# Performance work log

Hardware: AMD Instinct MI355X
Metric: run time of the kernel (lower is better)

Reference implementation:

```python
import jax, jax.numpy as jnp
import numpy as np

# IR-Net EDE surrogate-gradient constants (ir_1w1a.IRConv2d defaults)
K = 10.0
T = 0.1
BN_EPS = 1e-5

@jax.custom_vjp
def binary_quantize(x):
    return jnp.sign(x)

def _bq_fwd(x):
    return jnp.sign(x), x

def _bq_bwd(x, g):
    # grad = k * t * (1 - tanh(x*t)^2) * g   (IR-Net BinaryQuantize.backward)
    return (K * T * (1.0 - jnp.tanh(x * T) ** 2) * g,)

binary_quantize.defvjp(_bq_fwd, _bq_bwd)


def setup_inputs() -> dict:
    key = jax.random.key(0)
    k1, k2 = jax.random.split(key, 2)
    return {
        "x": jax.random.normal(k1, (32, 256, 56, 56), dtype=jnp.float32),
        "weight": jax.random.normal(k2, (256, 256, 3, 3), dtype=jnp.float32) * 0.05,
        "gamma": jnp.ones((256,), dtype=jnp.float32),
        "beta": jnp.zeros((256,), dtype=jnp.float32),
    }


def _convalg(x, weight, gamma, beta):
    co = weight.shape[0]
    wf = weight.reshape(co, -1)
    # per-output-channel standardization of weights
    bw = weight - wf.mean(-1).reshape(co, 1, 1, 1)
    std = jnp.std(bw.reshape(co, -1), axis=-1, ddof=1).reshape(co, 1, 1, 1)  # torch unbiased std
    bw = bw / std
    # detached power-of-2 per-channel scale: sw = 2^round(log2(mean|bw|))
    sw = jax.lax.stop_gradient(
        2.0 ** jnp.round(jnp.log2(jnp.abs(bw).reshape(co, -1).mean(-1)))
    ).reshape(co, 1, 1, 1)
    bwq = binary_quantize(bw) * sw   # binarized, scaled weights {-sw, +sw}
    ba = binary_quantize(x)          # binarized activations {-1, +1}
    y = jax.lax.conv_general_dilated(
        ba, bwq,
        window_strides=(1, 1),
        padding=((1, 1), (1, 1)),
        dimension_numbers=("NCHW", "OIHW", "NCHW"),
    )
    # BatchNorm2d, training-mode forward (batch statistics, biased variance)
    mean = y.mean(axis=(0, 2, 3), keepdims=True)
    var = y.var(axis=(0, 2, 3), keepdims=True)
    yn = (y - mean) * jax.lax.rsqrt(var + BN_EPS)
    yn = yn * gamma.reshape(1, -1, 1, 1) + beta.reshape(1, -1, 1, 1)
    # Hardtanh
    return jnp.clip(yn, -1.0, 1.0)


def reference(x, weight, gamma, beta):
    return _convalg(x, weight, gamma, beta)
```

## Files before the change

### kernel.cpp

```cpp
#include <hip/hip_runtime.h>
#include <math.h>

#define HH 56
#define WW 56
#define NB 32
#define CC 256
#define PIX 3136
#define M_TOT 100352
#define PADH 58
#define PADW 58
#define ACTQ_BYTES ((size_t)NB*PADH*PADW*CC)
#define WQ_BYTES ((size_t)9*CC*CC)
#define SBUF_BYTES ((size_t)M_TOT*CC*2)
#define BM 128
#define BN 128

typedef unsigned int u32;
typedef unsigned long long u64;
typedef int v4i __attribute__((ext_vector_type(4)));

typedef const __attribute__((address_space(1))) unsigned int* as1_u32p;
typedef __attribute__((address_space(3))) unsigned int* as3_u32p;
#define GLOAD_LDS16(g, l) \
  __builtin_amdgcn_global_load_lds((as1_u32p)(g), (as3_u32p)(l), 16, 0, 0)

__global__ __launch_bounds__(256) void pack_weights_i8(
    const float* __restrict__ wt, signed char* __restrict__ wq,
    float* __restrict__ swv,
    long long* __restrict__ sumS, long long* __restrict__ sumSS) {
  int co = blockIdx.x;
  int t  = threadIdx.x;
  int lane = t & 63, wid = t >> 6;

  float wv[9];
  const float* wp = wt + ((size_t)co*CC + t)*9;
  double psum = 0.0;
#pragma unroll
  for (int k = 0; k < 9; ++k) { wv[k] = wp[k]; psum += (double)wv[k]; }

  __shared__ double redm[4];
#pragma unroll
  for (int off = 32; off > 0; off >>= 1) psum += __shfl_xor(psum, off);
  if (lane == 0) redm[wid] = psum;
  __syncthreads();
  double mean = (redm[0]+redm[1]+redm[2]+redm[3]) * (1.0/2304.0);

  double pabs = 0.0, psq = 0.0;
#pragma unroll
  for (int k = 0; k < 9; ++k) {
    double d = (double)wv[k] - mean;
    pabs += fabs(d);
    psq  += d*d;
  }
#pragma unroll
  for (int off = 32; off > 0; off >>= 1) {
    pabs += __shfl_xor(pabs, off);
    psq  += __shfl_xor(psq,  off);
  }
  __shared__ double reda[4], redq[4];
  if (lane == 0) { reda[wid] = pabs; redq[wid] = psq; }
  __syncthreads();
  if (t == 0) {
    double sa = reda[0]+reda[1]+reda[2]+reda[3];
    double sq = redq[0]+redq[1]+redq[2]+redq[3];
    double stdv = sqrt(sq / 2303.0);
    double mabs = (sa * (1.0/2304.0)) / stdv;
    swv[co] = (float)exp2(rint(log2(mabs)));
    sumS[co]  = 0;
    sumSS[co] = 0;
  }
#pragma unroll
  for (int k = 0; k < 9; ++k)
    wq[((size_t)k*CC + co)*CC + t] =
        (((double)wv[k] - mean) > 0.0) ? (signed char)1 : (signed char)-1;
}

__global__ __launch_bounds__(256) void pack_acts_i8(
    const float* __restrict__ x, signed char* __restrict__ actq) {
  int n = blockIdx.y, tile = blockIdx.x;
  int lane = threadIdx.x & 63, cw = threadIdx.x >> 6;
  int pp = tile*64 + lane;
  if (pp >= PADH*PADW) return;
  int ph = pp / PADW, pw = pp - ph*PADW;
  signed char* dst = actq + ((size_t)(n*PADH + ph)*PADW + pw)*CC + cw*64;
  if (ph == 0 || ph == PADH-1 || pw == 0 || pw == PADW-1) {
    uint4 z = make_uint4(0u, 0u, 0u, 0u);
#pragma unroll
    for (int q = 0; q < 4; ++q) ((uint4*)dst)[q] = z;
    return;
  }
  int h = ph - 1, w = pw - 1;
  const float* xp = x + ((size_t)(n*CC + cw*64))*PIX + h*WW + w;
  u32 wrd[16];
#pragma unroll
  for (int c16 = 0; c16 < 16; ++c16) {
    u32 v = 0;
#pragma unroll
    for (int b = 0; b < 4; ++b) {
      float f = xp[(size_t)(c16*4 + b)*PIX];
      v |= (f > 0.0f ? 0x01u : 0xFFu) << (8*b);
    }
    wrd[c16] = v;
  }
#pragma unroll
  for (int q = 0; q < 4; ++q)
    ((uint4*)dst)[q] = make_uint4(wrd[4*q], wrd[4*q+1], wrd[4*q+2], wrd[4*q+3]);
}


#define STAGEM(SN, BUF) do {                                              \
    int tn_ = (SN) >> 2, kn_ = (SN) & 3;                                  \
    int aoff_ = ((tn_/3 - 1)*PADW + (tn_%3 - 1))*CC + kn_*64;             \
    int boff_ = tn_*65536 + kn_*64;                                       \
    char* nb_ = (char*)lds + (BUF)*16384;                                 \
    GLOAD_LDS16(pA0 + aoff_, nb_ + ldst);                                 \
    GLOAD_LDS16(pA1 + aoff_, nb_ + 4096 + ldst);                          \
    GLOAD_LDS16(pB0 + boff_, nb_ + 8192 + ldst);                          \
    GLOAD_LDS16(pB1 + boff_, nb_ + 12288 + ldst);                         \
  } while (0)

#define STEPM(S, BUF, WTXT, DOSTAGE) do {                                 \
    asm volatile("s_waitcnt " WTXT ::: "memory");                         \
    __builtin_amdgcn_s_barrier();                                         \
    const char* cb_ = (const char*)lds + (BUF)*16384;                     \
    v4i af[4], bf[4];                                                     \
    _Pragma("unroll")                                                     \
    for (int i = 0; i < 4; ++i)                                           \
      af[i] = *(const v4i*)(cb_ + (ar0 + i*16 + lm)*64 + rdo);            \
    _Pragma("unroll")                                                     \
    for (int j = 0; j < 4; ++j)                                           \
      bf[j] = *(const v4i*)(cb_ + 8192 + (bc0 + j*16 + lm)*64 + rdo);     \
    asm volatile("s_waitcnt lgkmcnt(0)" ::: "memory");                    \
    __builtin_amdgcn_s_barrier();                                         \
    if (DOSTAGE) { STAGEM((S) + 3, BUF); }                                \
    __builtin_amdgcn_s_setprio(1);                                        \
    _Pragma("unroll")                                                     \
    for (int i = 0; i < 4; ++i)                                           \
      _Pragma("unroll")                                                   \
      for (int j = 0; j < 4; ++j)                                         \
        acc[i][j] = __builtin_amdgcn_mfma_i32_16x16x64_i8(af[i], bf[j],   \
                                                          acc[i][j], 0, 0, 0); \
    __builtin_amdgcn_s_setprio(0);                                        \
  } while (0)

template <bool S16>
__global__ __launch_bounds__(256, 3) void bconv_mfma(
    const signed char* __restrict__ actq, const signed char* __restrict__ wq,
    short* __restrict__ s16out, float* __restrict__ f32out,
    u64* __restrict__ sumS, u64* __restrict__ sumSS) {
  __shared__ char lds[49152] __attribute__((aligned(16)));
  __shared__ int colS[128], colQ[128];

  int t = threadIdx.x;
  int lane = t & 63, wv = t >> 6;
  int lm = lane & 15, quad = lane >> 4;
  int ar0 = (wv & 1) * 64;
  int bc0 = (wv >> 1) * 64;
  int Mbase = blockIdx.x * BM;
  int n0 = blockIdx.y * BN;

  if (t < 128) { colS[t] = 0; colQ[t] = 0; }

  int r = t >> 2, c16 = t & 3;
  int cs = c16 ^ ((r >> 1) & 3);
  const signed char *pA0, *pA1;
  {
    int P = Mbase + r;
    int n_ = P / PIX, pl_ = P % PIX, h_ = pl_ / WW, w_ = pl_ % WW;
    pA0 = actq + ((size_t)(n_*PADH + h_+1)*PADW + (w_+1))*CC + cs*16;
    P += 64;
    n_ = P / PIX; pl_ = P % PIX; h_ = pl_ / WW; w_ = pl_ % WW;
    pA1 = actq + ((size_t)(n_*PADH + h_+1)*PADW + (w_+1))*CC + cs*16;
  }
  const signed char* pB0 = wq + (size_t)(n0 + r)*CC + cs*16;
  const signed char* pB1 = pB0 + 64*CC;
  int ldst = t*16;

  int rdo = (quad ^ ((lm >> 1) & 3)) * 16;

  v4i acc[4][4];
#pragma unroll
  for (int i = 0; i < 4; ++i)
#pragma unroll
    for (int j = 0; j < 4; ++j) acc[i][j] = 0;

  STAGEM(0, 0);
  STAGEM(1, 1);
  STAGEM(2, 2);

#pragma unroll 1
  for (int s = 0; s < 33; s += 3) {
    STEPM(s,     0, "vmcnt(8)", true);
    STEPM(s + 1, 1, "vmcnt(8)", true);
    STEPM(s + 2, 2, "vmcnt(8)", true);
  }
  STEPM(33, 0, "vmcnt(8)", false);
  STEPM(34, 1, "vmcnt(4)", false);
  STEPM(35, 2, "vmcnt(0)", false);

  int Sl[4] = {0,0,0,0}, Ql[4] = {0,0,0,0};
#pragma unroll
  for (int i = 0; i < 4; ++i) {
    int R = Mbase + ar0 + i*16 + quad*4;
    int nR = R / PIX, plR = R % PIX;
#pragma unroll
    for (int j = 0; j < 4; ++j) {
      int colo = n0 + bc0 + j*16 + lm;
      v4i a = acc[i][j];
      size_t idx = ((size_t)nR*CC + colo)*PIX + plR;
      if (S16) {
        int2 pk;
        pk.x = (a.x & 0xFFFF) | (a.y << 16);
        pk.y = (a.z & 0xFFFF) | (a.w << 16);
        *(int2*)(s16out + idx) = pk;
      } else {
        *(float4*)(f32out + idx) =
            make_float4((float)a.x, (float)a.y, (float)a.z, (float)a.w);
      }
      Sl[j] += a.x + a.y + a.z + a.w;
      Ql[j] += a.x*a.x + a.y*a.y + a.z*a.z + a.w*a.w;
    }
  }
#pragma unroll
  for (int j = 0; j < 4; ++j) {
    int S = Sl[j], Q = Ql[j];
    S += __shfl_xor(S, 16); S += __shfl_xor(S, 32);
    Q += __shfl_xor(Q, 16); Q += __shfl_xor(Q, 32);
    if (quad == 0) {
      atomicAdd(&colS[bc0 + j*16 + lm], S);
      atomicAdd(&colQ[bc0 + j*16 + lm], Q);
    }
  }
  __syncthreads();
  if (t < 128) {
    atomicAdd(&sumS[n0 + t], (u64)(long long)colS[t]);
    atomicAdd(&sumSS[n0 + t], (u64)(long long)colQ[t]);
  }
}

__global__ void finalize_stats(
    const long long* __restrict__ sumS, const long long* __restrict__ sumSS,
    const float* __restrict__ swv,
    const float* __restrict__ gamma, const float* __restrict__ beta,
    float* __restrict__ AB) {
  int c = threadIdx.x;
  double mu  = (double)sumS[c]  / (double)M_TOT;
  double var = (double)sumSS[c] / (double)M_TOT - mu*mu;
  double sw  = (double)swv[c];
  double inv = 1.0 / sqrt(sw*sw*var + 1e-5);
  double scale = (double)gamma[c] * sw * inv;
  double shift = (double)beta[c] - scale * mu;
  AB[c]      = (float)scale;
  AB[CC + c] = (float)shift;
}

__global__ __launch_bounds__(256) void bn_apply_s16(
    const short* __restrict__ s, float* __restrict__ out,
    const float* __restrict__ AB, int n8) {
  int i = blockIdx.x*256 + threadIdx.x;
  if (i >= n8) return;
  union { int4 v; short sh[8]; } u;
  u.v = ((const int4*)s)[i];
  int c = ((i*8) / PIX) & (CC-1);
  float a = AB[c], b = AB[CC + c];
  float4 o0, o1;
  o0.x = fminf(1.f, fmaxf(-1.f, (float)u.sh[0]*a + b));
  o0.y = fminf(1.f, fmaxf(-1.f, (float)u.sh[1]*a + b));
  o0.z = fminf(1.f, fmaxf(-1.f, (float)u.sh[2]*a + b));
  o0.w = fminf(1.f, fmaxf(-1.f, (float)u.sh[3]*a + b));
  o1.x = fminf(1.f, fmaxf(-1.f, (float)u.sh[4]*a + b));
  o1.y = fminf(1.f, fmaxf(-1.f, (float)u.sh[5]*a + b));
  o1.z = fminf(1.f, fmaxf(-1.f, (float)u.sh[6]*a + b));
  o1.w = fminf(1.f, fmaxf(-1.f, (float)u.sh[7]*a + b));
  ((float4*)out)[2*i]   = o0;
  ((float4*)out)[2*i+1] = o1;
}

__global__ __launch_bounds__(256) void bn_apply_f32(
    float* __restrict__ out, const float* __restrict__ AB, int n4) {
  int i = blockIdx.x*256 + threadIdx.x;
  if (i >= n4) return;
  float4 v = ((float4*)out)[i];
  int c = ((i*4) / PIX) & (CC-1);
  float a = AB[c], b = AB[CC + c];
  v.x = fminf(1.f, fmaxf(-1.f, v.x*a + b));
  v.y = fminf(1.f, fmaxf(-1.f, v.y*a + b));
  v.z = fminf(1.f, fmaxf(-1.f, v.z*a + b));
  v.w = fminf(1.f, fmaxf(-1.f, v.w*a + b));
  ((float4*)out)[i] = v;
}

extern "C" void kernel_launch(void* const* d_in, const int* in_sizes, int n_in,
                              void* d_out, int out_size, void* d_ws, size_t ws_size,
                              hipStream_t stream) {
  (void)in_sizes; (void)n_in; (void)out_size;
  const float* x     = (const float*)d_in[0];
  const float* wt    = (const float*)d_in[1];
  const float* gamma = (const float*)d_in[2];
  const float* beta  = (const float*)d_in[3];
  float* out = (float*)d_out;

  char* ws = (char*)d_ws;
  size_t off = 0;
  signed char* actq = (signed char*)(ws + off);
  off += ACTQ_BYTES;             off = (off + 255) & ~(size_t)255;
  signed char* wq = (signed char*)(ws + off);
  off += WQ_BYTES;               off = (off + 255) & ~(size_t)255;
  float* swv = (float*)(ws + off); off += 1024;
  float* AB  = (float*)(ws + off); off += 2048;
  long long* sumS  = (long long*)(ws + off); off += 2048;
  long long* sumSS = (long long*)(ws + off); off += 2048;
  off = (off + 255) & ~(size_t)255;
  short* sbuf = (short*)(ws + off);
  bool s16 = (ws_size >= off + SBUF_BYTES);

  pack_weights_i8<<<256, 256, 0, stream>>>(wt, wq, swv, sumS, sumSS);
  pack_acts_i8<<<dim3(53, NB), 256, 0, stream>>>(x, actq);
  if (s16) {
    bconv_mfma<true><<<dim3(M_TOT/BM, CC/BN), 256, 0, stream>>>(
        actq, wq, sbuf, nullptr, (u64*)sumS, (u64*)sumSS);
  } else {
    bconv_mfma<false><<<dim3(M_TOT/BM, CC/BN), 256, 0, stream>>>(
        actq, wq, nullptr, out, (u64*)sumS, (u64*)sumSS);
  }
  finalize_stats<<<1, 256, 0, stream>>>(sumS, sumSS, swv, gamma, beta, AB);
  if (s16) {
    bn_apply_s16<<<(M_TOT*CC/8 + 255)/256, 256, 0, stream>>>(
        sbuf, out, AB, M_TOT*CC/8);
  } else {
    bn_apply_f32<<<(M_TOT*CC/4 + 255)/256, 256, 0, stream>>>(
        out, AB, M_TOT*CC/4);
  }
}
```

Measured before the change: 162.0 us.

## Double-buffer MFMA register fragments to overlap LDS reads with MFMA

Restructures the main K-loop so each step reads the next stage's A/B fragments from LDS into a second register set while the MFMAs run on the current set. This removes one barrier per step and hides LDS read latency behind matrix math, with sched_barriers pinning the order. It costs extra VGPRs for the second fragment set, which may hurt occupancy under launch_bounds(256,3), and it changes the vmcnt wait accounting, which risks a race on the triple-buffered LDS.

```diff
diff --git a/kernel.cpp b/kernel.cpp
--- a/kernel.cpp
+++ b/kernel.cpp
@@ -119,28 +119,36 @@
     GLOAD_LDS16(pB1 + boff_, nb_ + 12288 + ldst);                         \
   } while (0)
 
-#define STEPM(S, BUF, WTXT, DOSTAGE) do {                                 \
+#define FRAGS_READ(NB_, NXTA, NXTB) do {                                  \
+    const char* cb_ = (const char*)lds + (NB_)*16384;                     \
+    _Pragma("unroll")                                                     \
+    for (int i_ = 0; i_ < 4; ++i_)                                        \
+      NXTA[i_] = *(const v4i*)(cb_ + (ar0 + i_*16 + lm)*64 + rdo);        \
+    _Pragma("unroll")                                                     \
+    for (int j_ = 0; j_ < 4; ++j_)                                        \
+      NXTB[j_] = *(const v4i*)(cb_ + 8192 + (bc0 + j_*16 + lm)*64 + rdo); \
+  } while (0)
+
+#define MFMA16(CURA, CURB) do {                                           \
+    __builtin_amdgcn_s_setprio(1);                                        \
+    _Pragma("unroll")                                                     \
+    for (int i_ = 0; i_ < 4; ++i_)                                        \
+      _Pragma("unroll")                                                   \
+      for (int j_ = 0; j_ < 4; ++j_)                                      \
+        acc[i_][j_] = __builtin_amdgcn_mfma_i32_16x16x64_i8(              \
+            CURA[i_], CURB[j_], acc[i_][j_], 0, 0, 0);                    \
+    __builtin_amdgcn_s_setprio(0);                                        \
+  } while (0)
+
+#define STEP(S, BUF, NBUF, CURA, CURB, NXTA, NXTB, WTXT, DOSTAGE) do {    \
     asm volatile("s_waitcnt " WTXT ::: "memory");                         \
     __builtin_amdgcn_s_barrier();                                         \
-    const char* cb_ = (const char*)lds + (BUF)*16384;                     \
-    v4i af[4], bf[4];                                                     \
-    _Pragma("unroll")                                                     \
-    for (int i = 0; i < 4; ++i)                                           \
-      af[i] = *(const v4i*)(cb_ + (ar0 + i*16 + lm)*64 + rdo);            \
-    _Pragma("unroll")                                                     \
-    for (int j = 0; j < 4; ++j)                                           \
-      bf[j] = *(const v4i*)(cb_ + 8192 + (bc0 + j*16 + lm)*64 + rdo);     \
+    __builtin_amdgcn_sched_barrier(0);                                    \
+    FRAGS_READ(NBUF, NXTA, NXTB);                                         \
+    if (DOSTAGE) { STAGEM((S) + 3, BUF); }                                \
+    MFMA16(CURA, CURB);                                                   \
     asm volatile("s_waitcnt lgkmcnt(0)" ::: "memory");                    \
-    __builtin_amdgcn_s_barrier();                                         \
-    if (DOSTAGE) { STAGEM((S) + 3, BUF); }                                \
-    __builtin_amdgcn_s_setprio(1);                                        \
-    _Pragma("unroll")                                                     \
-    for (int i = 0; i < 4; ++i)                                           \
-      _Pragma("unroll")                                                   \
-      for (int j = 0; j < 4; ++j)                                         \
-        acc[i][j] = __builtin_amdgcn_mfma_i32_16x16x64_i8(af[i], bf[j],   \
-                                                          acc[i][j], 0, 0, 0); \
-    __builtin_amdgcn_s_setprio(0);                                        \
+    __builtin_amdgcn_sched_barrier(0);                                    \
   } while (0)
 
 template <bool S16>
@@ -184,19 +192,33 @@
 #pragma unroll
     for (int j = 0; j < 4; ++j) acc[i][j] = 0;
 
+  v4i a0[4], b0[4], a1[4], b1[4];
+
   STAGEM(0, 0);
   STAGEM(1, 1);
   STAGEM(2, 2);
+  asm volatile("s_waitcnt vmcnt(8)" ::: "memory");
+  __builtin_amdgcn_s_barrier();
+  __builtin_amdgcn_sched_barrier(0);
+  FRAGS_READ(0, a0, b0);
+  asm volatile("s_waitcnt lgkmcnt(0)" ::: "memory");
+  __builtin_amdgcn_sched_barrier(0);
 
 #pragma unroll 1
-  for (int s = 0; s < 33; s += 3) {
-    STEPM(s,     0, "vmcnt(8)", true);
-    STEPM(s + 1, 1, "vmcnt(8)", true);
-    STEPM(s + 2, 2, "vmcnt(8)", true);
-  }
-  STEPM(33, 0, "vmcnt(8)", false);
-  STEPM(34, 1, "vmcnt(4)", false);
-  STEPM(35, 2, "vmcnt(0)", false);
+  for (int s6 = 0; s6 < 30; s6 += 6) {
+    STEP(s6+0, 0, 1, a0, b0, a1, b1, "vmcnt(4)", true);
+    STEP(s6+1, 1, 2, a1, b1, a0, b0, "vmcnt(4)", true);
+    STEP(s6+2, 2, 0, a0, b0, a1, b1, "vmcnt(4)", true);
+    STEP(s6+3, 0, 1, a1, b1, a0, b0, "vmcnt(4)", true);
+    STEP(s6+4, 1, 2, a0, b0, a1, b1, "vmcnt(4)", true);
+    STEP(s6+5, 2, 0, a1, b1, a0, b0, "vmcnt(4)", true);
+  }
+  STEP(30, 0, 1, a0, b0, a1, b1, "vmcnt(4)", true);
+  STEP(31, 1, 2, a1, b1, a0, b0, "vmcnt(4)", true);
+  STEP(32, 2, 0, a0, b0, a1, b1, "vmcnt(4)", true);
+  STEP(33, 0, 1, a1, b1, a0, b0, "vmcnt(4)", false);
+  STEP(34, 1, 2, a0, b0, a1, b1, "vmcnt(0)", false);
+  MFMA16(a1, b1);
 
   int Sl[4] = {0,0,0,0}, Ql[4] = {0,0,0,0};
 #pragma unroll
```

New measurement: 164.9 us. No clear change (+1.8%).

## Load weight fragments directly to registers and tile-major int16 intermediate layout

Applied to the files above, without the earlier changes.

The GEMM loop now stages only activations through LDS with a 3-slot ring and loads weight fragments straight from global memory into double-buffered registers. This drops the second barrier per step and halves LDS use. Occupancy hint drops from 3 to 2 blocks per CU. The int16 intermediate is written in a per-tile contiguous layout, and the BN apply kernel remaps indices back to NCHW, so the conv kernel's stores become contiguous while the scatter moves into the apply pass. Risks are uncoalesced direct weight loads, higher register pressure and a pipeline depth reduced from 3 stages to 2.

```diff
diff --git a/kernel.cpp b/kernel.cpp
--- a/kernel.cpp
+++ b/kernel.cpp
@@ -108,47 +108,50 @@
 }
 
 
-#define STAGEM(SN, BUF) do {                                              \
+#define STAGEA(SN) do {                                                   \
     int tn_ = (SN) >> 2, kn_ = (SN) & 3;                                  \
     int aoff_ = ((tn_/3 - 1)*PADW + (tn_%3 - 1))*CC + kn_*64;             \
-    int boff_ = tn_*65536 + kn_*64;                                       \
-    char* nb_ = (char*)lds + (BUF)*16384;                                 \
+    char* nb_ = (char*)lds + (((SN) % 3) << 13);                          \
     GLOAD_LDS16(pA0 + aoff_, nb_ + ldst);                                 \
     GLOAD_LDS16(pA1 + aoff_, nb_ + 4096 + ldst);                          \
-    GLOAD_LDS16(pB0 + boff_, nb_ + 8192 + ldst);                          \
-    GLOAD_LDS16(pB1 + boff_, nb_ + 12288 + ldst);                         \
   } while (0)
 
-#define STEPM(S, BUF, WTXT, DOSTAGE) do {                                 \
+#define LOADB(SN, BF) do {                                                \
+    int tn_ = (SN) >> 2, kn_ = (SN) & 3;                                  \
+    int boff_ = tn_*65536 + kn_*64;                                       \
+    BF[0] = *(const v4i*)(pBg + boff_);                                   \
+    BF[1] = *(const v4i*)(pBg + boff_ + 4096);                            \
+    BF[2] = *(const v4i*)(pBg + boff_ + 8192);                            \
+    BF[3] = *(const v4i*)(pBg + boff_ + 12288);                           \
+  } while (0)
+
+#define STEP(S, BCUR, BNXT, WTXT, DOA, DOB) do {                          \
     asm volatile("s_waitcnt " WTXT ::: "memory");                         \
     __builtin_amdgcn_s_barrier();                                         \
-    const char* cb_ = (const char*)lds + (BUF)*16384;                     \
-    v4i af[4], bf[4];                                                     \
+    __builtin_amdgcn_sched_barrier(0);                                    \
+    if (DOB) { LOADB((S) + 1, BNXT); }                                    \
+    if (DOA) { STAGEA((S) + 2); }                                         \
+    const char* cb_ = (const char*)lds + (((S) % 3) << 13);               \
+    v4i af[4];                                                            \
     _Pragma("unroll")                                                     \
-    for (int i = 0; i < 4; ++i)                                           \
-      af[i] = *(const v4i*)(cb_ + (ar0 + i*16 + lm)*64 + rdo);            \
-    _Pragma("unroll")                                                     \
-    for (int j = 0; j < 4; ++j)                                           \
-      bf[j] = *(const v4i*)(cb_ + 8192 + (bc0 + j*16 + lm)*64 + rdo);     \
-    asm volatile("s_waitcnt lgkmcnt(0)" ::: "memory");                    \
-    __builtin_amdgcn_s_barrier();                                         \
-    if (DOSTAGE) { STAGEM((S) + 3, BUF); }                                \
+    for (int i_ = 0; i_ < 4; ++i_)                                        \
+      af[i_] = *(const v4i*)(cb_ + (ar0 + i_*16 + lm)*64 + rdo);          \
     __builtin_amdgcn_s_setprio(1);                                        \
     _Pragma("unroll")                                                     \
-    for (int i = 0; i < 4; ++i)                                           \
+    for (int j_ = 0; j_ < 4; ++j_)                                        \
       _Pragma("unroll")                                                   \
-      for (int j = 0; j < 4; ++j)                                         \
-        acc[i][j] = __builtin_amdgcn_mfma_i32_16x16x64_i8(af[i], bf[j],   \
-                                                          acc[i][j], 0, 0, 0); \
+      for (int i_ = 0; i_ < 4; ++i_)                                      \
+        acc[i_][j_] = __builtin_amdgcn_mfma_i32_16x16x64_i8(              \
+            af[i_], BCUR[j_], acc[i_][j_], 0, 0, 0);                      \
     __builtin_amdgcn_s_setprio(0);                                        \
   } while (0)
 
 template <bool S16>
-__global__ __launch_bounds__(256, 3) void bconv_mfma(
+__global__ __launch_bounds__(256, 2) void bconv_mfma(
     const signed char* __restrict__ actq, const signed char* __restrict__ wq,
     short* __restrict__ s16out, float* __restrict__ f32out,
     u64* __restrict__ sumS, u64* __restrict__ sumSS) {
-  __shared__ char lds[49152] __attribute__((aligned(16)));
+  __shared__ char lds[24576] __attribute__((aligned(16)));
   __shared__ int colS[128], colQ[128];
 
   int t = threadIdx.x;
@@ -172,53 +175,73 @@
     n_ = P / PIX; pl_ = P % PIX; h_ = pl_ / WW; w_ = pl_ % WW;
     pA1 = actq + ((size_t)(n_*PADH + h_+1)*PADW + (w_+1))*CC + cs*16;
   }
-  const signed char* pB0 = wq + (size_t)(n0 + r)*CC + cs*16;
-  const signed char* pB1 = pB0 + 64*CC;
   int ldst = t*16;
 
   int rdo = (quad ^ ((lm >> 1) & 3)) * 16;
 
+  const signed char* pBg = wq + (size_t)(n0 + bc0 + lm)*CC + quad*16;
+
   v4i acc[4][4];
 #pragma unroll
   for (int i = 0; i < 4; ++i)
 #pragma unroll
     for (int j = 0; j < 4; ++j) acc[i][j] = 0;
 
-  STAGEM(0, 0);
-  STAGEM(1, 1);
-  STAGEM(2, 2);
+  v4i b0[4], b1[4];
+
+  STAGEA(0);
+  STAGEA(1);
+  LOADB(0, b0);
 
 #pragma unroll 1
-  for (int s = 0; s < 33; s += 3) {
-    STEPM(s,     0, "vmcnt(8)", true);
-    STEPM(s + 1, 1, "vmcnt(8)", true);
-    STEPM(s + 2, 2, "vmcnt(8)", true);
-  }
-  STEPM(33, 0, "vmcnt(8)", false);
-  STEPM(34, 1, "vmcnt(4)", false);
-  STEPM(35, 2, "vmcnt(0)", false);
+  for (int s6 = 0; s6 < 30; s6 += 6) {
+    STEP(s6+0, b0, b1, "vmcnt(6)", 1, 1);
+    STEP(s6+1, b1, b0, "vmcnt(6)", 1, 1);
+    STEP(s6+2, b0, b1, "vmcnt(6)", 1, 1);
+    STEP(s6+3, b1, b0, "vmcnt(6)", 1, 1);
+    STEP(s6+4, b0, b1, "vmcnt(6)", 1, 1);
+    STEP(s6+5, b1, b0, "vmcnt(6)", 1, 1);
+  }
+  STEP(30, b0, b1, "vmcnt(6)", 1, 1);
+  STEP(31, b1, b0, "vmcnt(6)", 1, 1);
+  STEP(32, b0, b1, "vmcnt(6)", 1, 1);
+  STEP(33, b1, b0, "vmcnt(6)", 1, 1);
+  STEP(34, b0, b1, "vmcnt(6)", 0, 1);
+  STEP(35, b1, b0, "vmcnt(4)", 0, 0);
 
   int Sl[4] = {0,0,0,0}, Ql[4] = {0,0,0,0};
-#pragma unroll
-  for (int i = 0; i < 4; ++i) {
-    int R = Mbase + ar0 + i*16 + quad*4;
-    int nR = R / PIX, plR = R % PIX;
-#pragma unroll
-    for (int j = 0; j < 4; ++j) {
-      int colo = n0 + bc0 + j*16 + lm;
-      v4i a = acc[i][j];
-      size_t idx = ((size_t)nR*CC + colo)*PIX + plR;
-      if (S16) {
+  if (S16) {
+    short* tb = s16out + ((size_t)(blockIdx.x*2 + blockIdx.y)) * (BM*BN);
+#pragma unroll
+    for (int i = 0; i < 4; ++i) {
+      int rhat = ar0 + i*16 + quad*4;
+#pragma unroll
+      for (int j = 0; j < 4; ++j) {
+        int colo = bc0 + j*16 + lm;
+        v4i a = acc[i][j];
         int2 pk;
         pk.x = (a.x & 0xFFFF) | (a.y << 16);
         pk.y = (a.z & 0xFFFF) | (a.w << 16);
-        *(int2*)(s16out + idx) = pk;
-      } else {
+        *(int2*)(tb + (size_t)colo*BM + rhat) = pk;
+        Sl[j] += a.x + a.y + a.z + a.w;
+        Ql[j] += a.x*a.x + a.y*a.y + a.z*a.z + a.w*a.w;
+      }
+    }
+  } else {
+#pragma unroll
+    for (int i = 0; i < 4; ++i) {
+      int R = Mbase + ar0 + i*16 + quad*4;
+      int nR = R / PIX, plR = R % PIX;
+#pragma unroll
+      for (int j = 0; j < 4; ++j) {
+        int colo = n0 + bc0 + j*16 + lm;
+        v4i a = acc[i][j];
+        size_t idx = ((size_t)nR*CC + colo)*PIX + plR;
         *(float4*)(f32out + idx) =
             make_float4((float)a.x, (float)a.y, (float)a.z, (float)a.w);
+        Sl[j] += a.x + a.y + a.z + a.w;
+        Ql[j] += a.x*a.x + a.y*a.y + a.z*a.z + a.w*a.w;
       }
-      Sl[j] += a.x + a.y + a.z + a.w;
-      Ql[j] += a.x*a.x + a.y*a.y + a.z*a.z + a.w*a.w;
     }
   }
 #pragma unroll
@@ -261,8 +284,17 @@
   if (i >= n8) return;
   union { int4 v; short sh[8]; } u;
   u.v = ((const int4*)s)[i];
-  int c = ((i*8) / PIX) & (CC-1);
-  float a = AB[c], b = AB[CC + c];
+  int base   = i*8;
+  int tile   = base >> 14;
+  int within = base & 16383;
+  int col7   = within >> 7;
+  int rh     = within & 127;
+  int bx = tile >> 1, cy = tile & 1;
+  int col = cy*BN + col7;
+  int R  = bx*BM + rh;
+  int n_ = R / PIX, pl = R % PIX;
+  float a = AB[col], b = AB[CC + col];
+  float* op = out + ((size_t)n_*CC + col)*PIX + pl;
   float4 o0, o1;
   o0.x = fminf(1.f, fmaxf(-1.f, (float)u.sh[0]*a + b));
   o0.y = fminf(1.f, fmaxf(-1.f, (float)u.sh[1]*a + b));
@@ -272,8 +304,8 @@
   o1.y = fminf(1.f, fmaxf(-1.f, (float)u.sh[5]*a + b));
   o1.z = fminf(1.f, fmaxf(-1.f, (float)u.sh[6]*a + b));
   o1.w = fminf(1.f, fmaxf(-1.f, (float)u.sh[7]*a + b));
-  ((float4*)out)[2*i]   = o0;
-  ((float4*)out)[2*i+1] = o1;
+  ((float4*)op)[0] = o0;
+  ((float4*)op)[1] = o1;
 }
 
 __global__ __launch_bounds__(256) void bn_apply_f32(
```

Result: slower. 220.9 us (+36.3%).
